# Performance work log

Hardware: AMD Instinct MI355X
Metric: run time of the kernel (lower is better)

## Reference

```python
import jax, jax.numpy as jnp
import numpy as np


def setup_inputs() -> dict:
    key = jax.random.key(0)
    k1, k2, k3, k4, k5 = jax.random.split(key, 5)
    B, S, T = 32, 2048, 512
    return {
        "unary_potentials": jax.random.normal(k1, (B, S, T), dtype=jnp.float32),
        "binary_potentials": jax.random.normal(k2, (T, T), dtype=jnp.float32),
        "tags": jax.random.randint(k3, (B, S), 0, T, dtype=jnp.int32),
        "predicted_tags": jax.random.randint(k4, (B, S), 0, T, dtype=jnp.int32),
        "mask": jax.random.randint(k5, (B, S), 0, 2, dtype=jnp.int32),
    }


def _score(unary, binary, tags, mask):
    # unary: [B,S,T], binary: [T,T], tags/mask: [B,S]
    B, S, T = unary.shape
    seq_len = jnp.sum(mask, axis=-1)              # [B]; original iterates range(sum(mask))
    pos = jnp.arange(S)
    valid = (pos[None, :] < seq_len[:, None]).astype(unary.dtype)      # [B,S]
    # unary score: unary[b, i, tags[b, i]] for i < seq_len
    un = jnp.take_along_axis(unary, tags[..., None], axis=2)[..., 0]   # [B,S]
    # transition score: binary[tags[b, i-1], tags[b, i]] for 1 <= i < seq_len
    tr = binary[tags[:, :-1], tags[:, 1:]]                             # [B,S-1]
    valid_tr = (pos[1:][None, :] < seq_len[:, None]).astype(unary.dtype)
    return jnp.sum(un * valid, axis=-1) + jnp.sum(tr * valid_tr, axis=-1)  # [B]


def reference(unary_potentials, binary_potentials, tags, predicted_tags, mask):
    gold = _score(unary_potentials, binary_potentials, tags, mask)
    pred = _score(unary_potentials, binary_potentials, predicted_tags, mask)
    losses = jnp.maximum(pred - gold, 0.0)
    return jnp.sum(losses)
```

## Files before the change

kernel.cpp:

```cpp
#include <hip/hip_runtime.h>


#define BB 32
#define SS 2048
#define TT 512

__device__ int sp_counter = 0;

__global__ __launch_bounds__(256) void sp_fused_kernel(
    const float* __restrict__ unary,
    const float* __restrict__ binary,
    const int*   __restrict__ tags,
    const int*   __restrict__ pred,
    const int*   __restrict__ mask,
    float*       __restrict__ ws,
    float*       __restrict__ out)
{
    const int b    = blockIdx.x;
    const int tid  = threadIdx.x;
    const int wave = tid >> 6;

    __shared__ int   s_ipart[4];
    __shared__ float s_part[8];
    __shared__ int   s_len;

    int m = 0;
    for (int s = tid; s < SS; s += 256) m += mask[b * SS + s];
    #pragma unroll
    for (int off = 32; off > 0; off >>= 1) m += __shfl_down(m, off);
    if ((tid & 63) == 0) s_ipart[wave] = m;
    __syncthreads();
    if (tid == 0) s_len = s_ipart[0] + s_ipart[1] + s_ipart[2] + s_ipart[3];
    __syncthreads();
    const int L = s_len;

    float g = 0.f, p = 0.f;
    for (int s = tid; s < SS; s += 256) {
        if (s < L) {
            const int base = b * SS + s;
            const int tg = tags[base];
            const int tp = pred[base];
            g += unary[base * TT + tg];
            p += unary[base * TT + tp];
            if (s >= 1) {
                const int tg0 = tags[base - 1];
                const int tp0 = pred[base - 1];
                g += binary[tg0 * TT + tg];
                p += binary[tp0 * TT + tp];
            }
        }
    }
    #pragma unroll
    for (int off = 32; off > 0; off >>= 1) {
        g += __shfl_down(g, off);
        p += __shfl_down(p, off);
    }
    if ((tid & 63) == 0) { s_part[wave * 2] = g; s_part[wave * 2 + 1] = p; }
    __syncthreads();

    if (tid == 0) {
        const float G = s_part[0] + s_part[2] + s_part[4] + s_part[6];
        const float P = s_part[1] + s_part[3] + s_part[5] + s_part[7];
        ws[2 * b]     = G;
        ws[2 * b + 1] = P;
        __threadfence();
        const int old = atomicAdd(&sp_counter, 1);
        if (old == BB - 1) {
            __threadfence();
            float total = 0.f;
            for (int i = 0; i < BB; ++i) {
                const float Gi = ws[2 * i];
                const float Pi = ws[2 * i + 1];
                total += fmaxf(Pi - Gi, 0.f);
            }
            out[0] = total;
            atomicExch(&sp_counter, 0);
        }
    }
}

extern "C" void kernel_launch(void* const* d_in, const int* in_sizes, int n_in,
                              void* d_out, int out_size, void* d_ws, size_t ws_size,
                              hipStream_t stream) {
    const float* unary  = (const float*)d_in[0];
    const float* binary = (const float*)d_in[1];
    const int*   tags   = (const int*)d_in[2];
    const int*   pred   = (const int*)d_in[3];
    const int*   mask   = (const int*)d_in[4];
    float* ws  = (float*)d_ws;
    float* out = (float*)d_out;

    sp_fused_kernel<<<BB, 256, 0, stream>>>(unary, binary, tags, pred, mask, ws, out);
}
```

Baseline: 12.53 us.

## Split each batch row across eight blocks and reduce the final loss in parallel

The grid grows from one block per batch row to eight blocks per row, so each thread handles a single sequence position and issues its tag and gather loads up front. With 256 blocks instead of 32, many more CUs can issue the scattered unary and binary gathers, hiding their latency. Each block still recomputes the full row mask sum, and the last-arriving block sums 256 partials and reduces the per-row hinge losses with a wave shuffle. The risk is extra redundant mask reads and more atomic traffic on the counter.

```diff
diff --git a/kernel.cpp b/kernel.cpp
--- a/kernel.cpp
+++ b/kernel.cpp
@@ -4,6 +4,8 @@
 #define BB 32
 #define SS 2048
 #define TT 512
+#define SLICES 8
+#define NBLK (BB * SLICES)
 
 __device__ int sp_counter = 0;
 
@@ -16,16 +18,27 @@
     float*       __restrict__ ws,
     float*       __restrict__ out)
 {
-    const int b    = blockIdx.x;
-    const int tid  = threadIdx.x;
-    const int wave = tid >> 6;
+    const int blk   = blockIdx.x;
+    const int b     = blk >> 3;
+    const int slice = blk & 7;
+    const int tid   = threadIdx.x;
+    const int wave  = tid >> 6;
+    const int s     = slice * 256 + tid;
+    const int base  = b * SS + s;
 
     __shared__ int   s_ipart[4];
     __shared__ float s_part[8];
     __shared__ int   s_len;
+    __shared__ int   s_last;
+
+    const int tg  = tags[base];
+    const int tp  = pred[base];
+    const int tg0 = (s >= 1) ? tags[base - 1] : 0;
+    const int tp0 = (s >= 1) ? pred[base - 1] : 0;
 
     int m = 0;
-    for (int s = tid; s < SS; s += 256) m += mask[b * SS + s];
+    #pragma unroll
+    for (int k = 0; k < 8; ++k) m += mask[b * SS + tid + k * 256];
     #pragma unroll
     for (int off = 32; off > 0; off >>= 1) m += __shfl_down(m, off);
     if ((tid & 63) == 0) s_ipart[wave] = m;
@@ -35,21 +48,15 @@
     const int L = s_len;
 
     float g = 0.f, p = 0.f;
-    for (int s = tid; s < SS; s += 256) {
-        if (s < L) {
-            const int base = b * SS + s;
-            const int tg = tags[base];
-            const int tp = pred[base];
-            g += unary[base * TT + tg];
-            p += unary[base * TT + tp];
-            if (s >= 1) {
-                const int tg0 = tags[base - 1];
-                const int tp0 = pred[base - 1];
-                g += binary[tg0 * TT + tg];
-                p += binary[tp0 * TT + tp];
-            }
+    if (s < L) {
+        g = unary[base * TT + tg];
+        p = unary[base * TT + tp];
+        if (s >= 1) {
+            g += binary[tg0 * TT + tg];
+            p += binary[tp0 * TT + tp];
         }
     }
+
     #pragma unroll
     for (int off = 32; off > 0; off >>= 1) {
         g += __shfl_down(g, off);
@@ -61,20 +68,30 @@
     if (tid == 0) {
         const float G = s_part[0] + s_part[2] + s_part[4] + s_part[6];
         const float P = s_part[1] + s_part[3] + s_part[5] + s_part[7];
-        ws[2 * b]     = G;
-        ws[2 * b + 1] = P;
+        ws[2 * blk]     = G;
+        ws[2 * blk + 1] = P;
         __threadfence();
         const int old = atomicAdd(&sp_counter, 1);
-        if (old == BB - 1) {
-            __threadfence();
-            float total = 0.f;
-            for (int i = 0; i < BB; ++i) {
-                const float Gi = ws[2 * i];
-                const float Pi = ws[2 * i + 1];
-                total += fmaxf(Pi - Gi, 0.f);
+        s_last = (old == NBLK - 1);
+    }
+    __syncthreads();
+
+    if (s_last) {
+        __threadfence();
+        if (tid < BB) {
+            float G = 0.f, P = 0.f;
+            #pragma unroll
+            for (int sl = 0; sl < SLICES; ++sl) {
+                G += ws[2 * (tid * SLICES + sl)];
+                P += ws[2 * (tid * SLICES + sl) + 1];
             }
-            out[0] = total;
-            atomicExch(&sp_counter, 0);
+            float loss = fmaxf(P - G, 0.f);
+            #pragma unroll
+            for (int off = 16; off > 0; off >>= 1) loss += __shfl_down(loss, off);
+            if (tid == 0) {
+                out[0] = loss;
+                atomicExch(&sp_counter, 0);
+            }
         }
     }
 }
@@ -90,5 +107,5 @@
     float* ws  = (float*)d_ws;
     float* out = (float*)d_out;
 
-    sp_fused_kernel<<<BB, 256, 0, stream>>>(unary, binary, tags, pred, mask, ws, out);
+    sp_fused_kernel<<<NBLK, 256, 0, stream>>>(unary, binary, tags, pred, mask, ws, out);
 }
```

New measurement: 14.03 us. 1.12x slower.

## Load tags, preds and mask once as int4 vectors and reuse neighbors via shuffles

Applied to the files above, without the earlier changes.

Each thread now owns 8 contiguous positions. It loads tags, predicted tags and mask with 128-bit vector loads a single time and keeps them in registers. The previous tag for a transition comes from the register array or from a wave shuffle, instead of a second global load. The 8-position gather loop is fully unrolled so the scattered unary and binary loads can be in flight together. This trades coalesced strided access for contiguous vector loads and raises register use per thread.

```diff
diff --git a/kernel.cpp b/kernel.cpp
--- a/kernel.cpp
+++ b/kernel.cpp
@@ -19,43 +19,63 @@
     const int b    = blockIdx.x;
     const int tid  = threadIdx.x;
     const int wave = tid >> 6;
+    const int lane = tid & 63;
 
     __shared__ int   s_ipart[4];
     __shared__ float s_part[8];
     __shared__ int   s_len;
 
-    int m = 0;
-    for (int s = tid; s < SS; s += 256) m += mask[b * SS + s];
+    const int s0   = tid * 8;
+    const int base = b * SS + s0;
+
+    const int4* tgp = reinterpret_cast<const int4*>(&tags[base]);
+    const int4* tpp = reinterpret_cast<const int4*>(&pred[base]);
+    const int4* mp  = reinterpret_cast<const int4*>(&mask[base]);
+    const int4 tgA = tgp[0], tgB = tgp[1];
+    const int4 tpA = tpp[0], tpB = tpp[1];
+    const int4 mA  = mp[0],  mB  = mp[1];
+
+    const int tg[8] = {tgA.x, tgA.y, tgA.z, tgA.w, tgB.x, tgB.y, tgB.z, tgB.w};
+    const int tp[8] = {tpA.x, tpA.y, tpA.z, tpA.w, tpB.x, tpB.y, tpB.z, tpB.w};
+
+    int prev_tg = __shfl_up(tg[7], 1);
+    int prev_tp = __shfl_up(tp[7], 1);
+    if (lane == 0 && s0 >= 1) {
+        prev_tg = tags[base - 1];
+        prev_tp = pred[base - 1];
+    }
+
+    int m = mA.x + mA.y + mA.z + mA.w + mB.x + mB.y + mB.z + mB.w;
     #pragma unroll
     for (int off = 32; off > 0; off >>= 1) m += __shfl_down(m, off);
-    if ((tid & 63) == 0) s_ipart[wave] = m;
+    if (lane == 0) s_ipart[wave] = m;
     __syncthreads();
     if (tid == 0) s_len = s_ipart[0] + s_ipart[1] + s_ipart[2] + s_ipart[3];
     __syncthreads();
     const int L = s_len;
 
     float g = 0.f, p = 0.f;
-    for (int s = tid; s < SS; s += 256) {
+    #pragma unroll
+    for (int k = 0; k < 8; ++k) {
+        const int s = s0 + k;
         if (s < L) {
-            const int base = b * SS + s;
-            const int tg = tags[base];
-            const int tp = pred[base];
-            g += unary[base * TT + tg];
-            p += unary[base * TT + tp];
+            g += unary[(base + k) * TT + tg[k]];
+            p += unary[(base + k) * TT + tp[k]];
             if (s >= 1) {
-                const int tg0 = tags[base - 1];
-                const int tp0 = pred[base - 1];
-                g += binary[tg0 * TT + tg];
-                p += binary[tp0 * TT + tp];
+                const int t0 = k ? tg[k - 1] : prev_tg;
+                const int q0 = k ? tp[k - 1] : prev_tp;
+                g += binary[t0 * TT + tg[k]];
+                p += binary[q0 * TT + tp[k]];
             }
         }
     }
+
     #pragma unroll
     for (int off = 32; off > 0; off >>= 1) {
         g += __shfl_down(g, off);
         p += __shfl_down(p, off);
     }
-    if ((tid & 63) == 0) { s_part[wave * 2] = g; s_part[wave * 2 + 1] = p; }
+    if (lane == 0) { s_part[wave * 2] = g; s_part[wave * 2 + 1] = p; }
     __syncthreads();
 
     if (tid == 0) {
```

New measurement: 15.56 us. 24.2% more time.
